# Optimization experiments

Hardware: AMD Instinct MI355X
Metric: run time of the kernel (lower is better)

The kernel has to match this reference:

```python
import jax, jax.numpy as jnp
import numpy as np

N = 50000      # num nodes
E = 800000     # num edges per edge set (before self loops)
F_IN = 256     # encoding_size
F_EMB = 256    # embedding_size
PE = 98        # d2an positional features (beijing)
ALPHA1 = 0.5
ALPHA2 = 0.5


def _uniform_linear(key, out_f, in_f):
    # torch.nn.Linear default init: U(-1/sqrt(in_f), 1/sqrt(in_f))
    s = 1.0 / np.sqrt(in_f)
    return jax.random.uniform(key, (out_f, in_f), jnp.float32, -s, s)


def setup_inputs() -> dict:
    key = jax.random.key(0)
    ks = jax.random.split(key, 18)
    inp = {
        'x': jax.random.normal(ks[0], (N, F_IN), jnp.float32),
        'd2an': jax.random.normal(ks[1], (N, PE), jnp.float32),
        'edge_index_l0': jax.random.randint(ks[2], (2, E), 0, N, jnp.int32),
        'edge_attr_l0': jax.random.uniform(ks[3], (E,), jnp.float32),
        'edge_index_l1': jax.random.randint(ks[4], (2, E), 0, N, jnp.int32),
        'edge_attr_l1': jax.random.uniform(ks[5], (E,), jnp.float32),
        # nodeLin of conv1/conv2 (used only on firstLayer with usePE)
        'Wnode1': _uniform_linear(ks[6], F_IN, F_IN + PE),
        'Wnode2': _uniform_linear(ks[7], F_IN, F_IN + PE),
        # lin1/lin2 of each conv layer (bias-free linears)
        'W11': _uniform_linear(ks[8], F_EMB, F_IN),
        'W12': _uniform_linear(ks[9], F_EMB, F_IN),
        'W21': _uniform_linear(ks[10], F_EMB, F_IN),
        'W22': _uniform_linear(ks[11], F_EMB, F_IN),
        'W31': _uniform_linear(ks[12], F_EMB, F_EMB),
        'W32': _uniform_linear(ks[13], F_EMB, F_EMB),
        'W41': _uniform_linear(ks[14], F_EMB, F_EMB),
        'W42': _uniform_linear(ks[15], F_EMB, F_EMB),
    }
    return inp


def _pos_knn_gnn_layer(x, row, col, attr, d2an, Wnode, W1, W2, first):
    """PosKnnGNNLayer.forward with useSI=True, usePE=True (eval mode).

    message = deg_norm * (x_j @ W1.T) + edge_norm * (x_j @ W2.T), scatter-add to col.
    Linearity lets us aggregate (norm * x_j) first, then apply W1/W2 once per node.
    """
    n = x.shape[0]
    loop = jnp.arange(n, dtype=row.dtype)
    row = jnp.concatenate([row, loop])          # source j
    col = jnp.concatenate([col, loop])          # target i
    attr = jnp.concatenate([attr, jnp.ones((n,), attr.dtype)])  # self-loop weight 1.0

    if first:
        x = jnp.concatenate([x, d2an], axis=1) @ Wnode.T  # [n, F_IN]

    deg = jax.ops.segment_sum(jnp.ones_like(attr), col, num_segments=n)
    dinv = jnp.where(deg > 0, deg ** -0.5, 0.0)
    deg_norm = dinv[row] * dinv[col]            # [E']

    einv = jnp.where(attr > 0, attr ** -0.5, 0.0)
    edge_norm = jnp.minimum(einv, 1.0)          # clamp values > 1.0 to 1.0

    xj = x[row]                                  # gather [E', F]
    a1 = jax.ops.segment_sum(deg_norm[:, None] * xj, col, num_segments=n)
    a2 = jax.ops.segment_sum(edge_norm[:, None] * xj, col, num_segments=n)
    return a1 @ W1.T + a2 @ W2.T                 # [n, F_EMB]


def reference(x, d2an, edge_index_l0, edge_attr_l0, edge_index_l1, edge_attr_l1,
              Wnode1, Wnode2, W11, W12, W21, W22, W31, W32, W41, W42):
    r0, c0 = edge_index_l0[0], edge_index_l0[1]
    r1, c1 = edge_index_l1[0], edge_index_l1[1]

    x0 = jax.nn.relu(_pos_knn_gnn_layer(x, r0, c0, edge_attr_l0, d2an, Wnode1, W11, W12, True))
    x1 = jax.nn.relu(_pos_knn_gnn_layer(x, r1, c1, edge_attr_l1, d2an, Wnode2, W21, W22, True))
    h = ALPHA1 * x0 + ALPHA2 * x1               # dropout p=0.3 is identity in eval

    x0 = jax.nn.relu(_pos_knn_gnn_layer(h, r0, c0, edge_attr_l0, None, None, W31, W32, False))
    x1 = jax.nn.relu(_pos_knn_gnn_layer(h, r1, c1, edge_attr_l1, None, None, W41, W42, False))
    return ALPHA1 * x0 + ALPHA2 * x1
```

## Files before the change

### kernel.cpp

```cpp
#include <hip/hip_runtime.h>


using bf16x8  = __attribute__((ext_vector_type(8))) __bf16;
using floatx4 = __attribute__((ext_vector_type(4))) float;
using f32x2   = __attribute__((ext_vector_type(2))) float;

__device__ __forceinline__ float b2f(unsigned short b) {
    return __uint_as_float(((unsigned)b) << 16);
}
__device__ __forceinline__ unsigned short f2b(float f) {
    unsigned u = __float_as_uint(f);
    return (unsigned short)((u + 0x7FFFu + ((u >> 16) & 1u)) >> 16);
}
__device__ __forceinline__ unsigned short f2h(float f) {
    _Float16 h = (_Float16)f;
    return __builtin_bit_cast(unsigned short, h);
}
__device__ __forceinline__ float h2f(unsigned short u) {
    return (float)__builtin_bit_cast(_Float16, u);
}


__global__ void k_cnt2(const int* __restrict__ col0, const int* __restrict__ col1,
                       int E, int* __restrict__ cnt0, int* __restrict__ cnt1) {
    int e = blockIdx.x * 256 + threadIdx.x;
    const int* col = blockIdx.y ? col1 : col0;
    int* cnt = blockIdx.y ? cnt1 : cnt0;
    if (e < E) atomicAdd(&cnt[col[e]], 1);
}

__global__ __launch_bounds__(1024) void k_scan2(
    const int* __restrict__ cnt0, const int* __restrict__ cnt1,
    int* __restrict__ off0, int* __restrict__ off1,
    int* __restrict__ cur0, int* __restrict__ cur1,
    float* __restrict__ dinv0, float* __restrict__ dinv1, int n) {
    const int* cnt = blockIdx.y ? cnt1 : cnt0;
    int* off = blockIdx.y ? off1 : off0;
    int* cur = blockIdx.y ? cur1 : cur0;
    float* dinv = blockIdx.y ? dinv1 : dinv0;
    __shared__ int wsum[16];
    __shared__ int wpre[16];
    __shared__ int carry;
    const int t = threadIdx.x;
    const int lane = t & 63;
    const int w = t >> 6;
    if (t == 0) { carry = 0; off[0] = 0; }
    __syncthreads();
    for (int base = 0; base < n; base += 1024) {
        int i = base + t;
        int raw = (i < n) ? cnt[i] : 0;
        int vpad = (raw + 7) & ~7;
        int v = vpad;
        #pragma unroll
        for (int d = 1; d < 64; d <<= 1) {
            int u = __shfl_up(v, d, 64);
            if (lane >= d) v += u;
        }
        if (lane == 63) wsum[w] = v;
        __syncthreads();
        if (t < 16) {
            int s = wsum[t];
            #pragma unroll
            for (int d = 1; d < 16; d <<= 1) {
                int u = __shfl_up(s, d, 16);
                if (t >= d) s += u;
            }
            wpre[t] = s;
        }
        __syncthreads();
        int add = carry + (w > 0 ? wpre[w - 1] : 0);
        if (i < n) {
            int incl = v + add;
            off[i + 1] = incl;
            cur[i] = incl - vpad;
            dinv[i] = rsqrtf((float)(raw + 1));
        }
        __syncthreads();
        if (t == 0) carry += wpre[15];
        __syncthreads();
    }
}

__global__ void k_fill2(const int* __restrict__ ei0, const float* __restrict__ ea0,
                        const int* __restrict__ ei1, const float* __restrict__ ea1,
                        int E, const float* __restrict__ dinv0,
                        const float* __restrict__ dinv1,
                        int* __restrict__ cur0, int* __restrict__ cur1,
                        uint2* __restrict__ rec0, uint2* __restrict__ rec1) {
    int e = blockIdx.x * 256 + threadIdx.x;
    if (e >= E) return;
    const int* ei = blockIdx.y ? ei1 : ei0;
    const float* ea = blockIdx.y ? ea1 : ea0;
    const float* dinv = blockIdx.y ? dinv1 : dinv0;
    int* cur = blockIdx.y ? cur1 : cur0;
    uint2* rec = blockIdx.y ? rec1 : rec0;
    int r = ei[e];
    int c = ei[E + e];
    float a = ea[e];
    float w2 = (a > 0.0f) ? fminf(rsqrtf(a), 1.0f) : 0.0f;
    float w1 = dinv[r] * dinv[c];
    int p = atomicAdd(&cur[c], 1);
    rec[p] = make_uint2((unsigned)r,
                        ((unsigned)f2h(w1) << 16) | (unsigned)f2h(w2));
}

__global__ void k_pad(const int* __restrict__ cnt0, const int* __restrict__ cnt1,
                      const int* __restrict__ off0, const int* __restrict__ off1,
                      uint2* __restrict__ rec0, uint2* __restrict__ rec1, int n) {
    int i = blockIdx.x * 256 + threadIdx.x;
    if (i >= n) return;
    const int* cnt = blockIdx.y ? cnt1 : cnt0;
    const int* off = blockIdx.y ? off1 : off0;
    uint2* rec = blockIdx.y ? rec1 : rec0;
    int p = off[i] + cnt[i], pe = off[i + 1];
    for (; p < pe; ++p) rec[p] = make_uint2(0u, 0u);
}


__global__ void k_xc(const float* __restrict__ x, const float* __restrict__ pe,
                     unsigned short* __restrict__ xc, int n, int F, int PEd,
                     int KC, int KP) {
    int idx = blockIdx.x * 256 + threadIdx.x;
    if (idx >= n * KP) return;
    int i = idx / KP, k = idx - i * KP;
    float v = 0.0f;
    if (k < F)        v = x[(size_t)i * F + k];
    else if (k < KC)  v = pe[(size_t)i * PEd + (k - F)];
    xc[idx] = f2b(v);
}

__global__ void k_wall(const float* __restrict__ Wn1, const float* __restrict__ Wn2,
                       const float* __restrict__ W11, const float* __restrict__ W12,
                       const float* __restrict__ W21, const float* __restrict__ W22,
                       const float* __restrict__ W31, const float* __restrict__ W32,
                       const float* __restrict__ W41, const float* __restrict__ W42,
                       unsigned short* __restrict__ wn0c, unsigned short* __restrict__ wn1c,
                       unsigned short* __restrict__ wc0, unsigned short* __restrict__ wc1,
                       unsigned short* __restrict__ wc2, unsigned short* __restrict__ wc3,
                       int F, int KC, int KP) {
    int idx = blockIdx.x * 256 + threadIdx.x;
    int npad = F * KP;
    if (idx < 2 * npad) {
        const float* W = (idx < npad) ? Wn1 : Wn2;
        unsigned short* Wc = (idx < npad) ? wn0c : wn1c;
        int t = (idx < npad) ? idx : idx - npad;
        int o = t / KP, k = t - o * KP;
        Wc[t] = f2b(k < KC ? W[(size_t)o * KC + k] : 0.0f);
        return;
    }
    int t = idx - 2 * npad;
    int seg = F * 512;
    if (t >= 4 * seg) return;
    int which = t / seg;
    int r = t - which * seg;
    const float* Wa = (which == 0) ? W11 : (which == 1) ? W21 : (which == 2) ? W31 : W41;
    const float* Wb = (which == 0) ? W12 : (which == 1) ? W22 : (which == 2) ? W32 : W42;
    unsigned short* Wc = (which == 0) ? wc0 : (which == 1) ? wc1 : (which == 2) ? wc2 : wc3;
    int o = r >> 9, k = r & 511;
    float v = (k < 256) ? Wa[(size_t)o * 256 + k] : Wb[(size_t)o * 256 + (k - 256)];
    Wc[r] = f2b(v);
}

__global__ __launch_bounds__(256) void k_agg(
    const unsigned short* __restrict__ X0, const unsigned short* __restrict__ X1,
    const int* __restrict__ off0, const int* __restrict__ off1,
    const uint2* __restrict__ rec0, const uint2* __restrict__ rec1,
    const float* __restrict__ dinv0, const float* __restrict__ dinv1,
    unsigned short* __restrict__ A0, unsigned short* __restrict__ A1, int n) {
    const int s = blockIdx.x & 1;
    const unsigned short* X = s ? X1 : X0;
    const int* off = s ? off1 : off0;
    const uint2* rec = s ? rec1 : rec0;
    const float* dinv = s ? dinv1 : dinv0;
    unsigned short* A = s ? A1 : A0;

    const int wave = threadIdx.x >> 6;
    const int lane = threadIdx.x & 63;
    const int gw = (blockIdx.x >> 1) * 4 + wave;
    if (gw >= n) return;

    const int e0 = __builtin_amdgcn_readfirstlane(off[gw]);
    const int e1 = __builtin_amdgcn_readfirstlane(off[gw + 1]);
    const float di = dinv[gw];
    const uint2* X2 = (const uint2*)X;
    uint2 xs = X2[(size_t)gw * 64 + lane];

    f32x2 a1lo = {0.f, 0.f}, a1hi = {0.f, 0.f};
    f32x2 a2lo = {0.f, 0.f}, a2hi = {0.f, 0.f};

    for (int base = e0; base < e1; base += 8) {
        uint2 rr[8];
        #pragma unroll
        for (int k = 0; k < 8; k++) rr[k] = rec[base + k];
        uint2 g[8];
        #pragma unroll
        for (int k = 0; k < 8; k++) {
            unsigned src = (unsigned)__builtin_amdgcn_readfirstlane(rr[k].x);
            g[k] = X2[(size_t)src * 64 + lane];
        }
        #pragma unroll
        for (int k = 0; k < 8; k++) {
            float w1 = h2f((unsigned short)(rr[k].y >> 16));
            float w2 = h2f((unsigned short)(rr[k].y & 0xFFFFu));
            f32x2 w1v = {w1, w1}, w2v = {w2, w2};
            f32x2 plo = {__uint_as_float(g[k].x << 16),
                         __uint_as_float(g[k].x & 0xFFFF0000u)};
            f32x2 phi = {__uint_as_float(g[k].y << 16),
                         __uint_as_float(g[k].y & 0xFFFF0000u)};
            a1lo += w1v * plo; a1hi += w1v * phi;
            a2lo += w2v * plo; a2hi += w2v * phi;
        }
    }

    {
        f32x2 plo = {__uint_as_float(xs.x << 16),
                     __uint_as_float(xs.x & 0xFFFF0000u)};
        f32x2 phi = {__uint_as_float(xs.y << 16),
                     __uint_as_float(xs.y & 0xFFFF0000u)};
        float ws = di * di;
        f32x2 wsv = {ws, ws};
        a1lo += wsv * plo; a1hi += wsv * phi;
        a2lo += plo;       a2hi += phi;
    }

    uint2 o1, o2;
    o1.x = (unsigned)f2b(a1lo.x) | ((unsigned)f2b(a1lo.y) << 16);
    o1.y = (unsigned)f2b(a1hi.x) | ((unsigned)f2b(a1hi.y) << 16);
    o2.x = (unsigned)f2b(a2lo.x) | ((unsigned)f2b(a2lo.y) << 16);
    o2.y = (unsigned)f2b(a2hi.x) | ((unsigned)f2b(a2hi.y) << 16);
    *(uint2*)(A + (size_t)gw * 512 + lane * 4) = o1;
    *(uint2*)(A + (size_t)gw * 512 + 256 + lane * 4) = o2;
}

#define GLL(g, l) \
    __builtin_amdgcn_global_load_lds((__attribute__((address_space(1))) void*)(g), \
                                     (__attribute__((address_space(3))) void*)(l), 16, 0, 0)

__global__ __launch_bounds__(256) void gemm_bt(
    const unsigned short* __restrict__ A,
    const unsigned short* __restrict__ B0, const unsigned short* __restrict__ B1,
    int M, int K, int Nc,
    unsigned short* __restrict__ outH0, unsigned short* __restrict__ outH1) {
    const unsigned short* B = blockIdx.z ? B1 : B0;
    unsigned short* outH = blockIdx.z ? outH1 : outH0;

    __shared__ __align__(16) unsigned short sA[128 * 32];
    __shared__ __align__(16) unsigned short sB[128 * 32];
    const int tid = threadIdx.x;
    const int lane = tid & 63;
    const int wave = tid >> 6;
    const int bm = blockIdx.x * 128;
    const int bn = blockIdx.y * 128;

    const int r0 = wave * 32 + (lane >> 2);
    const int kcol = (lane & 3) * 8;
    const int ga0 = min(bm + r0, M - 1);
    const int ga1 = min(bm + r0 + 16, M - 1);
    const int gb0 = min(bn + r0, Nc - 1);
    const int gb1 = min(bn + r0 + 16, Nc - 1);
    const unsigned short* pa0 = A + (size_t)ga0 * K + kcol;
    const unsigned short* pa1 = A + (size_t)ga1 * K + kcol;
    const unsigned short* pb0 = B + (size_t)gb0 * K + kcol;
    const unsigned short* pb1 = B + (size_t)gb1 * K + kcol;
    unsigned short* la0 = &sA[wave * 1024];
    unsigned short* la1 = &sA[wave * 1024 + 512];
    unsigned short* lb0 = &sB[wave * 1024];
    unsigned short* lb1 = &sB[wave * 1024 + 512];

    floatx4 acc[4][4];
    #pragma unroll
    for (int i = 0; i < 4; i++)
        #pragma unroll
        for (int j = 0; j < 4; j++) acc[i][j] = (floatx4){0.f, 0.f, 0.f, 0.f};

    const int mbase = (wave & 1) * 64 + (lane & 15);
    const int nbase = (wave >> 1) * 64 + (lane & 15);
    const int koff = (lane >> 4) * 8;

    for (int kk = 0; kk < K; kk += 32) {
        GLL(pa0 + kk, la0);
        GLL(pa1 + kk, la1);
        GLL(pb0 + kk, lb0);
        GLL(pb1 + kk, lb1);
        __syncthreads();
        bf16x8 af[4], bf[4];
        #pragma unroll
        for (int mi = 0; mi < 4; mi++)
            af[mi] = *(const bf16x8*)&sA[(mbase + mi * 16) * 32 + koff];
        #pragma unroll
        for (int ni = 0; ni < 4; ni++)
            bf[ni] = *(const bf16x8*)&sB[(nbase + ni * 16) * 32 + koff];
        #pragma unroll
        for (int mi = 0; mi < 4; mi++)
            #pragma unroll
            for (int ni = 0; ni < 4; ni++)
                acc[mi][ni] = __builtin_amdgcn_mfma_f32_16x16x32_bf16(
                    af[mi], bf[ni], acc[mi][ni], 0, 0, 0);
        __syncthreads();
    }

    const int crow = bm + (wave & 1) * 64 + (lane >> 4) * 4;
    const int ccol = bn + (wave >> 1) * 64 + (lane & 15);
    #pragma unroll
    for (int mi = 0; mi < 4; mi++)
        #pragma unroll
        for (int ni = 0; ni < 4; ni++)
            #pragma unroll
            for (int r = 0; r < 4; r++) {
                int row = crow + mi * 16 + r;
                if (row >= M) continue;
                int col = ccol + ni * 16;
                outH[(size_t)row * Nc + col] = f2b(acc[mi][ni][r]);
            }
}

__global__ __launch_bounds__(256) void gemm_dual(
    const unsigned short* __restrict__ A0, const unsigned short* __restrict__ B0,
    const unsigned short* __restrict__ A1, const unsigned short* __restrict__ B1,
    int M, int K, int Nc,
    float* __restrict__ outF, unsigned short* __restrict__ outH, float alpha) {
    __shared__ __align__(16) unsigned short sA[128 * 32];
    __shared__ __align__(16) unsigned short sB[128 * 32];
    const int tid = threadIdx.x;
    const int lane = tid & 63;
    const int wave = tid >> 6;
    const int bm = blockIdx.x * 128;
    const int bn = blockIdx.y * 128;

    const int r0 = wave * 32 + (lane >> 2);
    const int kcol = (lane & 3) * 8;
    const int ga0 = min(bm + r0, M - 1);
    const int ga1 = min(bm + r0 + 16, M - 1);
    const int gb0 = min(bn + r0, Nc - 1);
    const int gb1 = min(bn + r0 + 16, Nc - 1);
    unsigned short* la0 = &sA[wave * 1024];
    unsigned short* la1 = &sA[wave * 1024 + 512];
    unsigned short* lb0 = &sB[wave * 1024];
    unsigned short* lb1 = &sB[wave * 1024 + 512];

    const int mbase = (wave & 1) * 64 + (lane & 15);
    const int nbase = (wave >> 1) * 64 + (lane & 15);
    const int koff = (lane >> 4) * 8;

    floatx4 acc[4][4], res[4][4];

    #pragma unroll
    for (int pass = 0; pass < 2; pass++) {
        const unsigned short* A = pass ? A1 : A0;
        const unsigned short* B = pass ? B1 : B0;
        const unsigned short* pa0 = A + (size_t)ga0 * K + kcol;
        const unsigned short* pa1 = A + (size_t)ga1 * K + kcol;
        const unsigned short* pb0 = B + (size_t)gb0 * K + kcol;
        const unsigned short* pb1 = B + (size_t)gb1 * K + kcol;
        #pragma unroll
        for (int i = 0; i < 4; i++)
            #pragma unroll
            for (int j = 0; j < 4; j++) acc[i][j] = (floatx4){0.f, 0.f, 0.f, 0.f};

        for (int kk = 0; kk < K; kk += 32) {
            GLL(pa0 + kk, la0);
            GLL(pa1 + kk, la1);
            GLL(pb0 + kk, lb0);
            GLL(pb1 + kk, lb1);
            __syncthreads();
            bf16x8 af[4], bf[4];
            #pragma unroll
            for (int mi = 0; mi < 4; mi++)
                af[mi] = *(const bf16x8*)&sA[(mbase + mi * 16) * 32 + koff];
            #pragma unroll
            for (int ni = 0; ni < 4; ni++)
                bf[ni] = *(const bf16x8*)&sB[(nbase + ni * 16) * 32 + koff];
            #pragma unroll
            for (int mi = 0; mi < 4; mi++)
                #pragma unroll
                for (int ni = 0; ni < 4; ni++)
                    acc[mi][ni] = __builtin_amdgcn_mfma_f32_16x16x32_bf16(
                        af[mi], bf[ni], acc[mi][ni], 0, 0, 0);
            __syncthreads();
        }
        if (pass == 0) {
            #pragma unroll
            for (int mi = 0; mi < 4; mi++)
                #pragma unroll
                for (int ni = 0; ni < 4; ni++)
                    #pragma unroll
                    for (int r = 0; r < 4; r++)
                        res[mi][ni][r] = fmaxf(acc[mi][ni][r], 0.0f);
        }
    }

    const int crow = bm + (wave & 1) * 64 + (lane >> 4) * 4;
    const int ccol = bn + (wave >> 1) * 64 + (lane & 15);
    #pragma unroll
    for (int mi = 0; mi < 4; mi++)
        #pragma unroll
        for (int ni = 0; ni < 4; ni++)
            #pragma unroll
            for (int r = 0; r < 4; r++) {
                int row = crow + mi * 16 + r;
                if (row >= M) continue;
                int col = ccol + ni * 16;
                float v = alpha * (res[mi][ni][r] + fmaxf(acc[mi][ni][r], 0.0f));
                size_t idx = (size_t)row * Nc + col;
                if (outF) outF[idx] = v;
                else      outH[idx] = f2b(v);
            }
}


extern "C" void kernel_launch(void* const* d_in, const int* in_sizes, int n_in,
                              void* d_out, int out_size, void* d_ws, size_t ws_size,
                              hipStream_t stream) {
    const int F = 256;
    const int N = in_sizes[0] / F;
    const int PEd = in_sizes[1] / N;
    const int E = in_sizes[2] / 2;
    const int KC = F + PEd;
    const int KP = (KC + 31) & ~31;

    const float* x   = (const float*)d_in[0];
    const float* pe  = (const float*)d_in[1];
    const int*   ei0 = (const int*)d_in[2];
    const float* ea0 = (const float*)d_in[3];
    const int*   ei1 = (const int*)d_in[4];
    const float* ea1 = (const float*)d_in[5];
    const float* Wn1 = (const float*)d_in[6];
    const float* Wn2 = (const float*)d_in[7];
    const float* W11 = (const float*)d_in[8];
    const float* W12 = (const float*)d_in[9];
    const float* W21 = (const float*)d_in[10];
    const float* W22 = (const float*)d_in[11];
    const float* W31 = (const float*)d_in[12];
    const float* W32 = (const float*)d_in[13];
    const float* W41 = (const float*)d_in[14];
    const float* W42 = (const float*)d_in[15];
    float* out = (float*)d_out;

    char* p = (char*)d_ws;
    auto alloc = [&](size_t b) -> char* {
        char* r = p;
        p += (b + 255) & ~(size_t)255;
        return r;
    };
    int*   cnt01 = (int*)alloc((size_t)2 * N * 4);
    int*   cnt0  = cnt01;
    int*   cnt1  = cnt01 + N;
    int*   off0  = (int*)alloc((size_t)(N + 1) * 4);
    int*   off1  = (int*)alloc((size_t)(N + 1) * 4);
    int*   cur0  = (int*)alloc((size_t)N * 4);
    int*   cur1  = (int*)alloc((size_t)N * 4);
    float* dinv0 = (float*)alloc((size_t)N * 4);
    float* dinv1 = (float*)alloc((size_t)N * 4);
    uint2* rec0  = (uint2*)alloc(((size_t)E + 8ull * N) * 8);
    uint2* rec1  = (uint2*)alloc(((size_t)E + 8ull * N) * 8);
    unsigned short* wn0c = (unsigned short*)alloc((size_t)F * KP * 2);
    unsigned short* wn1c = (unsigned short*)alloc((size_t)F * KP * 2);
    unsigned short* wc0  = (unsigned short*)alloc((size_t)F * 512 * 2);
    unsigned short* wc1  = (unsigned short*)alloc((size_t)F * 512 * 2);
    unsigned short* wc2  = (unsigned short*)alloc((size_t)F * 512 * 2);
    unsigned short* wc3  = (unsigned short*)alloc((size_t)F * 512 * 2);
    unsigned short* xa   = (unsigned short*)alloc((size_t)N * 512 * 2);
    unsigned short* xb   = xa + (size_t)N * 256;
    unsigned short* h    = (unsigned short*)alloc((size_t)N * F * 2);
    unsigned short* a12  = (unsigned short*)alloc((size_t)N * 512 * 2);
    unsigned short* xc   = a12;
    unsigned short* a12bL1 = (unsigned short*)d_out;
    unsigned short* a12bL2 = xa;

    const int B = 256;
    const int gE = (E + B - 1) / B;
    const int gN = (N + B - 1) / B;
    const int gAgg = 2 * ((N + 3) / 4);
    dim3 gemm_grid((N + 127) / 128, 2);
    dim3 gemm_grid2((N + 127) / 128, 2, 2);

    hipMemsetAsync(cnt01, 0, (size_t)2 * N * 4, stream);
    k_cnt2<<<dim3(gE, 2), B, 0, stream>>>(ei0 + E, ei1 + E, E, cnt0, cnt1);
    k_scan2<<<dim3(1, 2), 1024, 0, stream>>>(cnt0, cnt1, off0, off1,
                                             cur0, cur1, dinv0, dinv1, N);
    k_fill2<<<dim3(gE, 2), B, 0, stream>>>(ei0, ea0, ei1, ea1, E, dinv0, dinv1,
                                           cur0, cur1, rec0, rec1);
    k_pad<<<dim3(gN, 2), B, 0, stream>>>(cnt0, cnt1, off0, off1, rec0, rec1, N);

    k_xc<<<((size_t)N * KP + B - 1) / B, B, 0, stream>>>(x, pe, xc, N, F, PEd, KC, KP);
    {
        int tot = 2 * F * KP + 4 * F * 512;
        k_wall<<<(tot + B - 1) / B, B, 0, stream>>>(Wn1, Wn2, W11, W12, W21, W22,
                                                    W31, W32, W41, W42,
                                                    wn0c, wn1c, wc0, wc1, wc2, wc3,
                                                    F, KC, KP);
    }

    gemm_bt<<<gemm_grid2, B, 0, stream>>>(xc, wn0c, wn1c, N, KP, F, xa, xb);

    k_agg<<<gAgg, B, 0, stream>>>(xa, xb, off0, off1, rec0, rec1,
                                  dinv0, dinv1, a12, a12bL1, N);
    gemm_dual<<<gemm_grid, B, 0, stream>>>(a12, wc0, a12bL1, wc1, N, 512, F,
                                           nullptr, h, 0.5f);

    k_agg<<<gAgg, B, 0, stream>>>(h, h, off0, off1, rec0, rec1,
                                  dinv0, dinv1, a12, a12bL2, N);
    gemm_dual<<<gemm_grid, B, 0, stream>>>(a12, wc2, a12bL2, wc3, N, 512, F,
                                           out, nullptr, 0.5f);
}
```

Baseline: 783.5 us.

## Compress edge records to 32 bits and merge fill and pad kernels

Each CSR edge record shrinks from 8 bytes to 4: a 16-bit source index plus an fp16 edge weight. The degree-norm weight is no longer stored; aggregation rebuilds it by loading dinv[src] and applying the destination's dinv once at the end. Padding entries are masked with the real edge count, the pad-fill work is folded into the fill kernel's launch, and the scan now handles four counts per thread. The aim is less record traffic and fewer launches, at the cost of an extra dinv gather per edge and a source index limited to 65536 nodes.

```diff
diff --git a/kernel.cpp b/kernel.cpp
--- a/kernel.cpp
+++ b/kernel.cpp
@@ -46,11 +46,20 @@
     const int w = t >> 6;
     if (t == 0) { carry = 0; off[0] = 0; }
     __syncthreads();
-    for (int base = 0; base < n; base += 1024) {
-        int i = base + t;
-        int raw = (i < n) ? cnt[i] : 0;
-        int vpad = (raw + 7) & ~7;
-        int v = vpad;
+    for (int base = 0; base < n; base += 4096) {
+        int i0 = base + t * 4;
+        int4 c = {0, 0, 0, 0};
+        if (i0 + 3 < n) {
+            c = *(const int4*)(cnt + i0);
+        } else if (i0 < n) {
+            c.x = cnt[i0];
+            if (i0 + 1 < n) c.y = cnt[i0 + 1];
+            if (i0 + 2 < n) c.z = cnt[i0 + 2];
+        }
+        int p0 = (c.x + 7) & ~7, p1 = (c.y + 7) & ~7;
+        int p2 = (c.z + 7) & ~7, p3 = (c.w + 7) & ~7;
+        int tot = p0 + p1 + p2 + p3;
+        int v = tot;
         #pragma unroll
         for (int d = 1; d < 64; d <<= 1) {
             int u = __shfl_up(v, d, 64);
@@ -68,12 +77,26 @@
             wpre[t] = s;
         }
         __syncthreads();
-        int add = carry + (w > 0 ? wpre[w - 1] : 0);
-        if (i < n) {
-            int incl = v + add;
-            off[i + 1] = incl;
-            cur[i] = incl - vpad;
-            dinv[i] = rsqrtf((float)(raw + 1));
+        int excl = (v - tot) + carry + (w > 0 ? wpre[w - 1] : 0);
+        if (i0 < n) {
+            off[i0 + 1] = excl + p0;
+            cur[i0] = excl;
+            dinv[i0] = rsqrtf((float)(c.x + 1));
+        }
+        if (i0 + 1 < n) {
+            off[i0 + 2] = excl + p0 + p1;
+            cur[i0 + 1] = excl + p0;
+            dinv[i0 + 1] = rsqrtf((float)(c.y + 1));
+        }
+        if (i0 + 2 < n) {
+            off[i0 + 3] = excl + p0 + p1 + p2;
+            cur[i0 + 2] = excl + p0 + p1;
+            dinv[i0 + 2] = rsqrtf((float)(c.z + 1));
+        }
+        if (i0 + 3 < n) {
+            off[i0 + 4] = excl + tot;
+            cur[i0 + 3] = excl + p0 + p1 + p2;
+            dinv[i0 + 3] = rsqrtf((float)(c.w + 1));
         }
         __syncthreads();
         if (t == 0) carry += wpre[15];
@@ -83,37 +106,34 @@
 
 __global__ void k_fill2(const int* __restrict__ ei0, const float* __restrict__ ea0,
                         const int* __restrict__ ei1, const float* __restrict__ ea1,
-                        int E, const float* __restrict__ dinv0,
-                        const float* __restrict__ dinv1,
+                        int E, int n, int gE,
+                        const int* __restrict__ cnt0, const int* __restrict__ cnt1,
+                        const int* __restrict__ off0, const int* __restrict__ off1,
                         int* __restrict__ cur0, int* __restrict__ cur1,
-                        uint2* __restrict__ rec0, uint2* __restrict__ rec1) {
-    int e = blockIdx.x * 256 + threadIdx.x;
-    if (e >= E) return;
-    const int* ei = blockIdx.y ? ei1 : ei0;
-    const float* ea = blockIdx.y ? ea1 : ea0;
-    const float* dinv = blockIdx.y ? dinv1 : dinv0;
-    int* cur = blockIdx.y ? cur1 : cur0;
-    uint2* rec = blockIdx.y ? rec1 : rec0;
-    int r = ei[e];
-    int c = ei[E + e];
-    float a = ea[e];
-    float w2 = (a > 0.0f) ? fminf(rsqrtf(a), 1.0f) : 0.0f;
-    float w1 = dinv[r] * dinv[c];
-    int p = atomicAdd(&cur[c], 1);
-    rec[p] = make_uint2((unsigned)r,
-                        ((unsigned)f2h(w1) << 16) | (unsigned)f2h(w2));
-}
-
-__global__ void k_pad(const int* __restrict__ cnt0, const int* __restrict__ cnt1,
-                      const int* __restrict__ off0, const int* __restrict__ off1,
-                      uint2* __restrict__ rec0, uint2* __restrict__ rec1, int n) {
-    int i = blockIdx.x * 256 + threadIdx.x;
-    if (i >= n) return;
-    const int* cnt = blockIdx.y ? cnt1 : cnt0;
-    const int* off = blockIdx.y ? off1 : off0;
-    uint2* rec = blockIdx.y ? rec1 : rec0;
-    int p = off[i] + cnt[i], pe = off[i + 1];
-    for (; p < pe; ++p) rec[p] = make_uint2(0u, 0u);
+                        unsigned* __restrict__ rec0, unsigned* __restrict__ rec1) {
+    const int by = blockIdx.y;
+    if (blockIdx.x < (unsigned)gE) {
+        int e = blockIdx.x * 256 + threadIdx.x;
+        if (e >= E) return;
+        const int* ei = by ? ei1 : ei0;
+        const float* ea = by ? ea1 : ea0;
+        int* cur = by ? cur1 : cur0;
+        unsigned* rec = by ? rec1 : rec0;
+        int r = ei[e];
+        int c = ei[E + e];
+        float a = ea[e];
+        float w2 = (a > 0.0f) ? fminf(rsqrtf(a), 1.0f) : 0.0f;
+        int p = atomicAdd(&cur[c], 1);
+        rec[p] = (unsigned)r | ((unsigned)f2h(w2) << 16);
+    } else {
+        int i = (blockIdx.x - gE) * 256 + threadIdx.x;
+        if (i >= n) return;
+        const int* cnt = by ? cnt1 : cnt0;
+        const int* off = by ? off1 : off0;
+        unsigned* rec = by ? rec1 : rec0;
+        int p = off[i] + cnt[i], pe2 = off[i + 1];
+        for (; p < pe2; ++p) rec[p] = 0u;
+    }
 }
 
 
@@ -164,13 +184,15 @@
 __global__ __launch_bounds__(256) void k_agg(
     const unsigned short* __restrict__ X0, const unsigned short* __restrict__ X1,
     const int* __restrict__ off0, const int* __restrict__ off1,
-    const uint2* __restrict__ rec0, const uint2* __restrict__ rec1,
+    const int* __restrict__ cnt0, const int* __restrict__ cnt1,
+    const unsigned* __restrict__ rec0, const unsigned* __restrict__ rec1,
     const float* __restrict__ dinv0, const float* __restrict__ dinv1,
     unsigned short* __restrict__ A0, unsigned short* __restrict__ A1, int n) {
     const int s = blockIdx.x & 1;
     const unsigned short* X = s ? X1 : X0;
     const int* off = s ? off1 : off0;
-    const uint2* rec = s ? rec1 : rec0;
+    const int* cnt = s ? cnt1 : cnt0;
+    const unsigned* rec = s ? rec1 : rec0;
     const float* dinv = s ? dinv1 : dinv0;
     unsigned short* A = s ? A1 : A0;
 
@@ -181,6 +203,7 @@
 
     const int e0 = __builtin_amdgcn_readfirstlane(off[gw]);
     const int e1 = __builtin_amdgcn_readfirstlane(off[gw + 1]);
+    const int rend = e0 + __builtin_amdgcn_readfirstlane(cnt[gw]);
     const float di = dinv[gw];
     const uint2* X2 = (const uint2*)X;
     uint2 xs = X2[(size_t)gw * 64 + lane];
@@ -189,26 +212,28 @@
     f32x2 a2lo = {0.f, 0.f}, a2hi = {0.f, 0.f};
 
     for (int base = e0; base < e1; base += 8) {
-        uint2 rr[8];
-        #pragma unroll
-        for (int k = 0; k < 8; k++) rr[k] = rec[base + k];
+        float ds[8], w2[8];
         uint2 g[8];
         #pragma unroll
         for (int k = 0; k < 8; k++) {
-            unsigned src = (unsigned)__builtin_amdgcn_readfirstlane(rr[k].x);
-            g[k] = X2[(size_t)src * 64 + lane];
+            unsigned rr = __builtin_amdgcn_readfirstlane(rec[base + k]);
+            int srck = (int)(rr & 0xFFFFu);
+            bool val = (base + k) < rend;
+            float dk = dinv[srck];
+            float wk = h2f((unsigned short)(rr >> 16));
+            ds[k] = val ? dk : 0.0f;
+            w2[k] = val ? wk : 0.0f;
+            g[k] = X2[(size_t)srck * 64 + lane];
         }
         #pragma unroll
         for (int k = 0; k < 8; k++) {
-            float w1 = h2f((unsigned short)(rr[k].y >> 16));
-            float w2 = h2f((unsigned short)(rr[k].y & 0xFFFFu));
-            f32x2 w1v = {w1, w1}, w2v = {w2, w2};
+            f32x2 dv = {ds[k], ds[k]}, wv = {w2[k], w2[k]};
             f32x2 plo = {__uint_as_float(g[k].x << 16),
                          __uint_as_float(g[k].x & 0xFFFF0000u)};
             f32x2 phi = {__uint_as_float(g[k].y << 16),
                          __uint_as_float(g[k].y & 0xFFFF0000u)};
-            a1lo += w1v * plo; a1hi += w1v * phi;
-            a2lo += w2v * plo; a2hi += w2v * phi;
+            a1lo += dv * plo; a1hi += dv * phi;
+            a2lo += wv * plo; a2hi += wv * phi;
         }
     }
 
@@ -217,10 +242,11 @@
                      __uint_as_float(xs.x & 0xFFFF0000u)};
         f32x2 phi = {__uint_as_float(xs.y << 16),
                      __uint_as_float(xs.y & 0xFFFF0000u)};
-        float ws = di * di;
-        f32x2 wsv = {ws, ws};
-        a1lo += wsv * plo; a1hi += wsv * phi;
-        a2lo += plo;       a2hi += phi;
+        f32x2 dv = {di, di};
+        a1lo = dv * (a1lo + dv * plo);
+        a1hi = dv * (a1hi + dv * phi);
+        a2lo += plo;
+        a2hi += phi;
     }
 
     uint2 o1, o2;
@@ -451,8 +477,8 @@
     int*   cur1  = (int*)alloc((size_t)N * 4);
     float* dinv0 = (float*)alloc((size_t)N * 4);
     float* dinv1 = (float*)alloc((size_t)N * 4);
-    uint2* rec0  = (uint2*)alloc(((size_t)E + 8ull * N) * 8);
-    uint2* rec1  = (uint2*)alloc(((size_t)E + 8ull * N) * 8);
+    unsigned* rec0 = (unsigned*)alloc(((size_t)E + 8ull * N) * 4);
+    unsigned* rec1 = (unsigned*)alloc(((size_t)E + 8ull * N) * 4);
     unsigned short* wn0c = (unsigned short*)alloc((size_t)F * KP * 2);
     unsigned short* wn1c = (unsigned short*)alloc((size_t)F * KP * 2);
     unsigned short* wc0  = (unsigned short*)alloc((size_t)F * 512 * 2);
@@ -478,9 +504,9 @@
     k_cnt2<<<dim3(gE, 2), B, 0, stream>>>(ei0 + E, ei1 + E, E, cnt0, cnt1);
     k_scan2<<<dim3(1, 2), 1024, 0, stream>>>(cnt0, cnt1, off0, off1,
                                              cur0, cur1, dinv0, dinv1, N);
-    k_fill2<<<dim3(gE, 2), B, 0, stream>>>(ei0, ea0, ei1, ea1, E, dinv0, dinv1,
-                                           cur0, cur1, rec0, rec1);
-    k_pad<<<dim3(gN, 2), B, 0, stream>>>(cnt0, cnt1, off0, off1, rec0, rec1, N);
+    k_fill2<<<dim3(gE + gN, 2), B, 0, stream>>>(ei0, ea0, ei1, ea1, E, N, gE,
+                                                cnt0, cnt1, off0, off1,
+                                                cur0, cur1, rec0, rec1);
 
     k_xc<<<((size_t)N * KP + B - 1) / B, B, 0, stream>>>(x, pe, xc, N, F, PEd, KC, KP);
     {
@@ -493,12 +519,12 @@
 
     gemm_bt<<<gemm_grid2, B, 0, stream>>>(xc, wn0c, wn1c, N, KP, F, xa, xb);
 
-    k_agg<<<gAgg, B, 0, stream>>>(xa, xb, off0, off1, rec0, rec1,
+    k_agg<<<gAgg, B, 0, stream>>>(xa, xb, off0, off1, cnt0, cnt1, rec0, rec1,
                                   dinv0, dinv1, a12, a12bL1, N);
     gemm_dual<<<gemm_grid, B, 0, stream>>>(a12, wc0, a12bL1, wc1, N, 512, F,
                                            nullptr, h, 0.5f);
 
-    k_agg<<<gAgg, B, 0, stream>>>(h, h, off0, off1, rec0, rec1,
+    k_agg<<<gAgg, B, 0, stream>>>(h, h, off0, off1, cnt0, cnt1, rec0, rec1,
                                   dinv0, dinv1, a12, a12bL2, N);
     gemm_dual<<<gemm_grid, B, 0, stream>>>(a12, wc2, a12bL2, wc3, N, 512, F,
                                            out, nullptr, 0.5f);
```

New measurement: 794.9 us. Within noise of the previous version (+1.5%).
